# Performance work log

Measured on AMD Instinct MI355X. Metric: run time of the kernel, lower is better.

## Reference

```python
import jax, jax.numpy as jnp
import numpy as np

LATENT = 3
HIDDEN = 16
INP = LATENT + 1  # prev_z cat action
B = 1048576


def setup_inputs() -> dict:
    key = jax.random.key(0)
    ks = jax.random.split(key, 11)
    s_ih = 1.0 / np.sqrt(HIDDEN)
    return {
        "prev_z": jax.random.normal(ks[0], (B, LATENT), jnp.float32),
        "action": jax.random.normal(ks[1], (B, 1), jnp.float32),
        "prev_h": jax.random.normal(ks[2], (B, HIDDEN), jnp.float32),
        # GRUCell params (torch layout: [3*H, in] and [3*H, H], gate order r,z,n)
        "W_ih": jax.random.uniform(ks[3], (3 * HIDDEN, INP), jnp.float32, -s_ih, s_ih),
        "W_hh": jax.random.uniform(ks[4], (3 * HIDDEN, HIDDEN), jnp.float32, -s_ih, s_ih),
        "b_ih": jax.random.uniform(ks[5], (3 * HIDDEN,), jnp.float32, -s_ih, s_ih),
        "b_hh": jax.random.uniform(ks[6], (3 * HIDDEN,), jnp.float32, -s_ih, s_ih),
        # prior heads
        "W_mu": jax.random.uniform(ks[7], (LATENT, HIDDEN), jnp.float32, -s_ih, s_ih),
        "b_mu": jax.random.uniform(ks[8], (LATENT,), jnp.float32, -s_ih, s_ih),
        "W_lv": jax.random.uniform(ks[9], (LATENT, HIDDEN), jnp.float32, -s_ih, s_ih),
        "b_lv": jax.random.uniform(ks[10], (LATENT,), jnp.float32, -s_ih, s_ih),
    }


def reference(prev_z, action, prev_h, W_ih, W_hh, b_ih, b_hh, W_mu, b_mu, W_lv, b_lv):
    x = jnp.concatenate([prev_z, action], axis=-1)              # [B, 4]
    gi = x @ W_ih.T + b_ih                                       # [B, 3H]
    gh = prev_h @ W_hh.T + b_hh                                  # [B, 3H]
    i_r, i_z, i_n = jnp.split(gi, 3, axis=-1)
    h_r, h_z, h_n = jnp.split(gh, 3, axis=-1)
    r = jax.nn.sigmoid(i_r + h_r)
    z = jax.nn.sigmoid(i_z + h_z)
    n = jnp.tanh(i_n + r * h_n)
    h = (1.0 - z) * n + z * prev_h                               # [B, H]
    mu = h @ W_mu.T + b_mu                                       # [B, 3]
    logvar = jnp.clip(h @ W_lv.T + b_lv, -5.0, 5.0)              # [B, 3]
    return mu, logvar, h
```

## Files before the change

kernel.cpp:

```cpp
#include <hip/hip_runtime.h>

#define TPB 256
#define WPT 4
#define ROW_DW 20
#define LDS_ROW_F32 (64 * ROW_DW)
#define LDS_MU_F32 192
#define LDS_WAVE_F32 (LDS_ROW_F32 + 2 * LDS_MU_F32)

typedef _Float16 half8 __attribute__((ext_vector_type(8)));
typedef __fp16  fp16x2 __attribute__((ext_vector_type(2)));
typedef float f32x4 __attribute__((ext_vector_type(4)));

__device__ __forceinline__ float fast_sigmoid(float x) {
    return __builtin_amdgcn_rcpf(1.0f + __expf(-x));
}
__device__ __forceinline__ float fast_tanh(float x) {
    return 2.0f * __builtin_amdgcn_rcpf(1.0f + __expf(-2.0f * x)) - 1.0f;
}
__device__ __forceinline__ half8 pack8(float4 lo, float4 hi) {
    union { fp16x2 p[4]; half8 h; } u;
    u.p[0] = __builtin_amdgcn_cvt_pkrtz(lo.x, lo.y);
    u.p[1] = __builtin_amdgcn_cvt_pkrtz(lo.z, lo.w);
    u.p[2] = __builtin_amdgcn_cvt_pkrtz(hi.x, hi.y);
    u.p[3] = __builtin_amdgcn_cvt_pkrtz(hi.z, hi.w);
    return u.h;
}


__global__ __launch_bounds__(64) void prep_kernel(
    const float* __restrict__ W_ih, const float* __restrict__ W_hh,
    const float* __restrict__ b_ih, const float* __restrict__ b_hh,
    const float* __restrict__ W_mu, const float* __restrict__ b_mu,
    const float* __restrict__ W_lv, const float* __restrict__ b_lv,
    void* __restrict__ wsv)
{
    _Float16* wsB = (_Float16*)wsv;
    const int l = threadIdx.x;
    const int col = l & 15, kg = l >> 4;

    #pragma unroll
    for (int t = 0; t < 4; ++t) {
        const int gate = (t == 0) ? col : (t == 1) ? (16 + col) : (32 + col);
        #pragma unroll
        for (int i = 0; i < 8; ++i) {
            const int k = kg * 8 + i;
            float v = 0.f;
            if (t <= 1) {
                if (k < 4)       v = W_ih[gate * 4 + k];
                else if (k < 20) v = W_hh[gate * 16 + (k - 4)];
            } else if (t == 2) {
                if (k < 4)       v = W_ih[gate * 4 + k];
            } else {
                if (k >= 4 && k < 20) v = W_hh[gate * 16 + (k - 4)];
            }
            wsB[t * 512 + l * 8 + i] = (_Float16)v;
        }
    }
    #pragma unroll
    for (int i = 0; i < 8; ++i) {
        const int k = kg * 8 + i;
        wsB[4 * 512 + l * 8 + i] = (_Float16)((k == col + 4) ? 1.f : 0.f);
    }
    #pragma unroll
    for (int i = 0; i < 8; ++i) {
        const int k = kg * 8 + i;
        const int m = col;
        float v = 0.f;
        if (m < 3) {
            if (k < 16)       v = W_mu[m * 16 + k];
            else if (k == 20) v = b_mu[m];
        } else if (m < 6) {
            if (k < 16)       v = W_lv[(m - 3) * 16 + k];
            else if (k == 20) v = b_lv[m - 3];
        }
        wsB[5 * 512 + l * 8 + i] = (_Float16)v;
    }
    if (l < 16) {
        float4* b4 = (float4*)((char*)wsv + 6144);
        b4[l] = make_float4(b_ih[l] + b_hh[l],
                            b_ih[16 + l] + b_hh[16 + l],
                            b_ih[32 + l],
                            b_hh[32 + l]);
    }
}

__global__ __launch_bounds__(TPB) void rssm_kernel(
    const float* __restrict__ prev_z,
    const float* __restrict__ action,
    const float* __restrict__ prev_h,
    const void*  __restrict__ wsv,
    float* __restrict__ out_mu,
    float* __restrict__ out_lv,
    float* __restrict__ out_h,
    int B)
{
    __shared__ float lds[4][LDS_WAVE_F32];
    const int tid = threadIdx.x;
    const int wid = tid >> 6, lane = tid & 63;
    const int col = lane & 15, kg = lane >> 4;
    const int wbase = (blockIdx.x * 4 + wid) * 64;
    if (wbase >= B) return;

    float* W  = lds[wid];
    float* MU = W + LDS_ROW_F32;
    float* LV = MU + LDS_MU_F32;

    const half8* Bp = (const half8*)wsv;
    const half8 bR  = Bp[lane];
    const half8 bZ  = Bp[64 + lane];
    const half8 bNi = Bp[128 + lane];
    const half8 bNh = Bp[192 + lane];
    const half8 bHp = Bp[256 + lane];
    const half8 a2  = Bp[320 + lane];
    const float4 bias = ((const float4*)((const char*)wsv + 6144))[col];

    {
        const float4* hg = (const float4*)prev_h;
        #pragma unroll
        for (int i = 0; i < 4; ++i) {
            const int fi = i * 64 + lane;
            const int r = fi >> 2, w = fi & 3;
            const int gi = min(wbase * 4 + fi, B * 4 - 1);
            const float4 v = hg[gi];
            *(float4*)&W[r * ROW_DW + 4 + w * 4] = v;
        }
        const int zr = min(wbase + lane, B - 1);
        const float z0 = prev_z[zr * 3 + 0];
        const float z1 = prev_z[zr * 3 + 1];
        const float z2 = prev_z[zr * 3 + 2];
        const float ac = action[zr];
        *(float4*)&W[lane * ROW_DW] = make_float4(z0, z1, z2, ac);
    }

    #pragma unroll
    for (int t = 0; t < WPT; ++t) {
        const float* ap = &W[(t * 16 + col) * ROW_DW + kg * 8];
        const float4 z4 = make_float4(0.f, 0.f, 0.f, 0.f);
        const float4 p0 = (kg < 3) ? *(const float4*)ap : z4;
        const float4 p1 = (kg < 2) ? *(const float4*)(ap + 4) : z4;
        const half8 a = pack8(p0, p1);

        f32x4 accR  = {bias.x, bias.x, bias.x, bias.x};
        f32x4 accZ  = {bias.y, bias.y, bias.y, bias.y};
        f32x4 accNi = {bias.z, bias.z, bias.z, bias.z};
        f32x4 accNh = {bias.w, bias.w, bias.w, bias.w};
        f32x4 accHp = {0.f, 0.f, 0.f, 0.f};
        accR  = __builtin_amdgcn_mfma_f32_16x16x32_f16(a, bR,  accR,  0, 0, 0);
        accZ  = __builtin_amdgcn_mfma_f32_16x16x32_f16(a, bZ,  accZ,  0, 0, 0);
        accNi = __builtin_amdgcn_mfma_f32_16x16x32_f16(a, bNi, accNi, 0, 0, 0);
        accNh = __builtin_amdgcn_mfma_f32_16x16x32_f16(a, bNh, accNh, 0, 0, 0);
        accHp = __builtin_amdgcn_mfma_f32_16x16x32_f16(a, bHp, accHp, 0, 0, 0);

        #pragma unroll
        for (int q = 0; q < 4; ++q) {
            const float r  = fast_sigmoid(accR[q]);
            const float z  = fast_sigmoid(accZ[q]);
            const float n  = fast_tanh(fmaf(r, accNh[q], accNi[q]));
            const float hv = fmaf(z, accHp[q] - n, n);
            W[(t * 16 + kg * 4 + q) * ROW_DW + 4 + col] = hv;
        }

        half8 b2;
        if (kg < 2) {
            const float* hr = &W[(t * 16 + col) * ROW_DW + 4 + kg * 8];
            b2 = pack8(*(const float4*)hr, *(const float4*)(hr + 4));
        } else {
            #pragma unroll
            for (int i = 0; i < 8; ++i) b2[i] = (_Float16)0.f;
            if (kg == 2) b2[4] = (_Float16)1.0f;
        }
        f32x4 acc2 = {0.f, 0.f, 0.f, 0.f};
        acc2 = __builtin_amdgcn_mfma_f32_16x16x32_f16(a2, b2, acc2, 0, 0, 0);

        const int mr = (t * 16 + col) * 3;
        if (kg == 0) {
            MU[mr + 0] = acc2[0];
            MU[mr + 1] = acc2[1];
            MU[mr + 2] = acc2[2];
            LV[mr + 0] = fminf(fmaxf(acc2[3], -5.0f), 5.0f);
        } else if (kg == 1) {
            LV[mr + 1] = fminf(fmaxf(acc2[0], -5.0f), 5.0f);
            LV[mr + 2] = fminf(fmaxf(acc2[1], -5.0f), 5.0f);
        }

        {
            const int r = lane >> 2, w = lane & 3;
            const float4 hv4 = *(const float4*)&W[(t * 16 + r) * ROW_DW + 4 + w * 4];
            const int orow = wbase + t * 16 + r;
            if (orow < B)
                *(float4*)&out_h[(size_t)orow * 16 + w * 4] = hv4;
        }
    }

    if (lane < 48) {
        const int gi = wbase * 3 + lane * 4;
        if (gi + 3 < B * 3) {
            *(float4*)&out_mu[gi] = *(const float4*)&MU[lane * 4];
            *(float4*)&out_lv[gi] = *(const float4*)&LV[lane * 4];
        }
    }
}

extern "C" void kernel_launch(void* const* d_in, const int* in_sizes, int n_in,
                              void* d_out, int out_size, void* d_ws, size_t ws_size,
                              hipStream_t stream) {
    const float* prev_z = (const float*)d_in[0];
    const float* action = (const float*)d_in[1];
    const float* prev_h = (const float*)d_in[2];
    const float* W_ih   = (const float*)d_in[3];
    const float* W_hh   = (const float*)d_in[4];
    const float* b_ih   = (const float*)d_in[5];
    const float* b_hh   = (const float*)d_in[6];
    const float* W_mu   = (const float*)d_in[7];
    const float* b_mu   = (const float*)d_in[8];
    const float* W_lv   = (const float*)d_in[9];
    const float* b_lv   = (const float*)d_in[10];

    const int B = in_sizes[0] / 3;
    float* out    = (float*)d_out;
    float* out_mu = out;
    float* out_lv = out + (size_t)3 * B;
    float* out_h  = out + (size_t)6 * B;

    prep_kernel<<<1, 64, 0, stream>>>(W_ih, W_hh, b_ih, b_hh,
                                      W_mu, b_mu, W_lv, b_lv, d_ws);

    const int rows_per_block = 256;
    const int blocks = (B + rows_per_block - 1) / rows_per_block;
    rssm_kernel<<<blocks, TPB, 0, stream>>>(prev_z, action, prev_h, d_ws,
                                            out_mu, out_lv, out_h, B);
}
```

Measured before the change: 42.95 us.

## Use persistent grid-stride waves with register prefetch of next chunk

Replaces the one-chunk-per-wave launch with a fixed grid of 1024 blocks whose waves loop over 64-row chunks in grid-stride order. While the current chunk is computed, the inputs for the next chunk (prev_h, prev_z, action) are prefetched into registers, so global load latency overlaps with MFMA and activation work and per-wave setup such as loading weights is amortized. The trade-off is higher register pressure and less parallelism from oversubscription, since each wave now runs its chunks serially.

Result: slower. 57.96 us (+35.0%).

```diff
diff --git a/kernel.cpp b/kernel.cpp
--- a/kernel.cpp
+++ b/kernel.cpp
@@ -6,6 +6,7 @@
 #define LDS_ROW_F32 (64 * ROW_DW)
 #define LDS_MU_F32 192
 #define LDS_WAVE_F32 (LDS_ROW_F32 + 2 * LDS_MU_F32)
+#define NBLOCKS 1024
 
 typedef _Float16 half8 __attribute__((ext_vector_type(8)));
 typedef __fp16  fp16x2 __attribute__((ext_vector_type(2)));
@@ -98,8 +99,6 @@
     const int tid = threadIdx.x;
     const int wid = tid >> 6, lane = tid & 63;
     const int col = lane & 15, kg = lane >> 4;
-    const int wbase = (blockIdx.x * 4 + wid) * 64;
-    if (wbase >= B) return;
 
     float* W  = lds[wid];
     float* MU = W + LDS_ROW_F32;
@@ -114,90 +113,116 @@
     const half8 a2  = Bp[320 + lane];
     const float4 bias = ((const float4*)((const char*)wsv + 6144))[col];
 
+    const int stride = NBLOCKS * 4;
+    int chunk = blockIdx.x * 4 + wid;
+    if (chunk * 64 >= B) return;
+
+    const float4* hg = (const float4*)prev_h;
+
+    float4 hreg[4], xar;
     {
-        const float4* hg = (const float4*)prev_h;
+        const int cb4 = chunk * 256;
+        #pragma unroll
+        for (int i = 0; i < 4; ++i)
+            hreg[i] = hg[min(cb4 + i * 64 + lane, B * 4 - 1)];
+        const int zr = min(chunk * 64 + lane, B - 1);
+        xar = make_float4(prev_z[zr * 3 + 0], prev_z[zr * 3 + 1],
+                          prev_z[zr * 3 + 2], action[zr]);
+    }
+
+    while (true) {
+        const int cbase = chunk * 64;
+
         #pragma unroll
         for (int i = 0; i < 4; ++i) {
             const int fi = i * 64 + lane;
             const int r = fi >> 2, w = fi & 3;
-            const int gi = min(wbase * 4 + fi, B * 4 - 1);
-            const float4 v = hg[gi];
-            *(float4*)&W[r * ROW_DW + 4 + w * 4] = v;
-        }
-        const int zr = min(wbase + lane, B - 1);
-        const float z0 = prev_z[zr * 3 + 0];
-        const float z1 = prev_z[zr * 3 + 1];
-        const float z2 = prev_z[zr * 3 + 2];
-        const float ac = action[zr];
-        *(float4*)&W[lane * ROW_DW] = make_float4(z0, z1, z2, ac);
-    }
-
-    #pragma unroll
-    for (int t = 0; t < WPT; ++t) {
-        const float* ap = &W[(t * 16 + col) * ROW_DW + kg * 8];
-        const float4 z4 = make_float4(0.f, 0.f, 0.f, 0.f);
-        const float4 p0 = (kg < 3) ? *(const float4*)ap : z4;
-        const float4 p1 = (kg < 2) ? *(const float4*)(ap + 4) : z4;
-        const half8 a = pack8(p0, p1);
-
-        f32x4 accR  = {bias.x, bias.x, bias.x, bias.x};
-        f32x4 accZ  = {bias.y, bias.y, bias.y, bias.y};
-        f32x4 accNi = {bias.z, bias.z, bias.z, bias.z};
-        f32x4 accNh = {bias.w, bias.w, bias.w, bias.w};
-        f32x4 accHp = {0.f, 0.f, 0.f, 0.f};
-        accR  = __builtin_amdgcn_mfma_f32_16x16x32_f16(a, bR,  accR,  0, 0, 0);
-        accZ  = __builtin_amdgcn_mfma_f32_16x16x32_f16(a, bZ,  accZ,  0, 0, 0);
-        accNi = __builtin_amdgcn_mfma_f32_16x16x32_f16(a, bNi, accNi, 0, 0, 0);
-        accNh = __builtin_amdgcn_mfma_f32_16x16x32_f16(a, bNh, accNh, 0, 0, 0);
-        accHp = __builtin_amdgcn_mfma_f32_16x16x32_f16(a, bHp, accHp, 0, 0, 0);
-
-        #pragma unroll
-        for (int q = 0; q < 4; ++q) {
-            const float r  = fast_sigmoid(accR[q]);
-            const float z  = fast_sigmoid(accZ[q]);
-            const float n  = fast_tanh(fmaf(r, accNh[q], accNi[q]));
-            const float hv = fmaf(z, accHp[q] - n, n);
-            W[(t * 16 + kg * 4 + q) * ROW_DW + 4 + col] = hv;
-        }
-
-        half8 b2;
-        if (kg < 2) {
-            const float* hr = &W[(t * 16 + col) * ROW_DW + 4 + kg * 8];
-            b2 = pack8(*(const float4*)hr, *(const float4*)(hr + 4));
-        } else {
+            *(float4*)&W[r * ROW_DW + 4 + w * 4] = hreg[i];
+        }
+        *(float4*)&W[lane * ROW_DW] = xar;
+
+        const int nchunk = chunk + stride;
+        const bool have_next = (nchunk * 64 < B);
+        if (have_next) {
+            const int cb4 = nchunk * 256;
             #pragma unroll
-            for (int i = 0; i < 8; ++i) b2[i] = (_Float16)0.f;
-            if (kg == 2) b2[4] = (_Float16)1.0f;
-        }
-        f32x4 acc2 = {0.f, 0.f, 0.f, 0.f};
-        acc2 = __builtin_amdgcn_mfma_f32_16x16x32_f16(a2, b2, acc2, 0, 0, 0);
-
-        const int mr = (t * 16 + col) * 3;
-        if (kg == 0) {
-            MU[mr + 0] = acc2[0];
-            MU[mr + 1] = acc2[1];
-            MU[mr + 2] = acc2[2];
-            LV[mr + 0] = fminf(fmaxf(acc2[3], -5.0f), 5.0f);
-        } else if (kg == 1) {
-            LV[mr + 1] = fminf(fmaxf(acc2[0], -5.0f), 5.0f);
-            LV[mr + 2] = fminf(fmaxf(acc2[1], -5.0f), 5.0f);
-        }
-
-        {
-            const int r = lane >> 2, w = lane & 3;
-            const float4 hv4 = *(const float4*)&W[(t * 16 + r) * ROW_DW + 4 + w * 4];
-            const int orow = wbase + t * 16 + r;
-            if (orow < B)
-                *(float4*)&out_h[(size_t)orow * 16 + w * 4] = hv4;
-        }
-    }
-
-    if (lane < 48) {
-        const int gi = wbase * 3 + lane * 4;
-        if (gi + 3 < B * 3) {
-            *(float4*)&out_mu[gi] = *(const float4*)&MU[lane * 4];
-            *(float4*)&out_lv[gi] = *(const float4*)&LV[lane * 4];
-        }
+            for (int i = 0; i < 4; ++i)
+                hreg[i] = hg[min(cb4 + i * 64 + lane, B * 4 - 1)];
+            const int zr = min(nchunk * 64 + lane, B - 1);
+            xar = make_float4(prev_z[zr * 3 + 0], prev_z[zr * 3 + 1],
+                              prev_z[zr * 3 + 2], action[zr]);
+        }
+
+        #pragma unroll
+        for (int t = 0; t < WPT; ++t) {
+            const float* ap = &W[(t * 16 + col) * ROW_DW + kg * 8];
+            const float4 z4 = make_float4(0.f, 0.f, 0.f, 0.f);
+            const float4 p0 = (kg < 3) ? *(const float4*)ap : z4;
+            const float4 p1 = (kg < 2) ? *(const float4*)(ap + 4) : z4;
+            const half8 a = pack8(p0, p1);
+
+            f32x4 accR  = {bias.x, bias.x, bias.x, bias.x};
+            f32x4 accZ  = {bias.y, bias.y, bias.y, bias.y};
+            f32x4 accNi = {bias.z, bias.z, bias.z, bias.z};
+            f32x4 accNh = {bias.w, bias.w, bias.w, bias.w};
+            f32x4 accHp = {0.f, 0.f, 0.f, 0.f};
+            accR  = __builtin_amdgcn_mfma_f32_16x16x32_f16(a, bR,  accR,  0, 0, 0);
+            accZ  = __builtin_amdgcn_mfma_f32_16x16x32_f16(a, bZ,  accZ,  0, 0, 0);
+            accNi = __builtin_amdgcn_mfma_f32_16x16x32_f16(a, bNi, accNi, 0, 0, 0);
+            accNh = __builtin_amdgcn_mfma_f32_16x16x32_f16(a, bNh, accNh, 0, 0, 0);
+            accHp = __builtin_amdgcn_mfma_f32_16x16x32_f16(a, bHp, accHp, 0, 0, 0);
+
+            #pragma unroll
+            for (int q = 0; q < 4; ++q) {
+                const float r  = fast_sigmoid(accR[q]);
+                const float z  = fast_sigmoid(accZ[q]);
+                const float n  = fast_tanh(fmaf(r, accNh[q], accNi[q]));
+                const float hv = fmaf(z, accHp[q] - n, n);
+                W[(t * 16 + kg * 4 + q) * ROW_DW + 4 + col] = hv;
+            }
+
+            half8 b2;
+            if (kg < 2) {
+                const float* hr = &W[(t * 16 + col) * ROW_DW + 4 + kg * 8];
+                b2 = pack8(*(const float4*)hr, *(const float4*)(hr + 4));
+            } else {
+                #pragma unroll
+                for (int i = 0; i < 8; ++i) b2[i] = (_Float16)0.f;
+                if (kg == 2) b2[4] = (_Float16)1.0f;
+            }
+            f32x4 acc2 = {0.f, 0.f, 0.f, 0.f};
+            acc2 = __builtin_amdgcn_mfma_f32_16x16x32_f16(a2, b2, acc2, 0, 0, 0);
+
+            const int mr = (t * 16 + col) * 3;
+            if (kg == 0) {
+                MU[mr + 0] = acc2[0];
+                MU[mr + 1] = acc2[1];
+                MU[mr + 2] = acc2[2];
+                LV[mr + 0] = fminf(fmaxf(acc2[3], -5.0f), 5.0f);
+            } else if (kg == 1) {
+                LV[mr + 1] = fminf(fmaxf(acc2[0], -5.0f), 5.0f);
+                LV[mr + 2] = fminf(fmaxf(acc2[1], -5.0f), 5.0f);
+            }
+
+            {
+                const int r = lane >> 2, w = lane & 3;
+                const float4 hv4 = *(const float4*)&W[(t * 16 + r) * ROW_DW + 4 + w * 4];
+                const int orow = cbase + t * 16 + r;
+                if (orow < B)
+                    *(float4*)&out_h[(size_t)orow * 16 + w * 4] = hv4;
+            }
+        }
+
+        if (lane < 48) {
+            const int gi = cbase * 3 + lane * 4;
+            if (gi + 3 < B * 3) {
+                *(float4*)&out_mu[gi] = *(const float4*)&MU[lane * 4];
+                *(float4*)&out_lv[gi] = *(const float4*)&LV[lane * 4];
+            }
+        }
+
+        if (!have_next) break;
+        chunk = nchunk;
     }
 }
 
@@ -225,8 +250,10 @@
     prep_kernel<<<1, 64, 0, stream>>>(W_ih, W_hh, b_ih, b_hh,
                                       W_mu, b_mu, W_lv, b_lv, d_ws);
 
-    const int rows_per_block = 256;
-    const int blocks = (B + rows_per_block - 1) / rows_per_block;
+    const int total_chunks = (B + 63) / 64;
+    int blocks = NBLOCKS;
+    if (total_chunks < NBLOCKS * 4)
+        blocks = (total_chunks + 3) / 4;
     rssm_kernel<<<blocks, TPB, 0, stream>>>(prev_z, action, prev_h, d_ws,
                                             out_mu, out_lv, out_h, B);
 }
```
